# Optimization experiments

Measured on AMD Instinct MI355X. Metric: run time of the kernel, lower is better.

## Reference

```python
import jax, jax.numpy as jnp
import numpy as np

B, H, W, DIM, HEADS, WS, SHIFT, MLP_RATIO = 32, 56, 56, 256, 8, 7, 3, 4
N = WS * WS                      # tokens per window = 49
NW = (H // WS) * (W // WS)       # windows per image = 64
HEAD_DIM = DIM // HEADS
HIDDEN = DIM * MLP_RATIO


def _rel_index():
    # standard Swin relative position index, shape (N, N), values in [0, (2*WS-1)^2)
    coords = np.stack(np.meshgrid(np.arange(WS), np.arange(WS), indexing='ij')).reshape(2, -1)
    rel = (coords[:, :, None] - coords[:, None, :]).transpose(1, 2, 0)
    rel[:, :, 0] += WS - 1
    rel[:, :, 1] += WS - 1
    rel[:, :, 0] *= 2 * WS - 1
    return rel.sum(-1).astype(np.int32)


def _attn_mask():
    # shifted-window attention mask, shape (NW, N, N), values in {0, -100}
    img = np.zeros((H, W))
    slices = (slice(0, -WS), slice(-WS, -SHIFT), slice(-SHIFT, None))
    cnt = 0
    for hs in slices:
        for ws_ in slices:
            img[hs, ws_] = cnt
            cnt += 1
    mw = img.reshape(H // WS, WS, W // WS, WS).transpose(0, 2, 1, 3).reshape(-1, N)
    diff = mw[:, None, :] - mw[:, :, None]
    return np.where(diff != 0, -100.0, 0.0).astype(np.float32)


def setup_inputs() -> dict:
    key = jax.random.key(0)
    ks = jax.random.split(key, 16)
    s = 0.02
    return {
        'x': jax.random.normal(ks[0], (B, H * W, DIM), jnp.float32),
        'norm1_w': jnp.ones((DIM,), jnp.float32),
        'norm1_b': jnp.zeros((DIM,), jnp.float32),
        'qkv_w': jax.random.normal(ks[1], (3 * DIM, DIM), jnp.float32) * s,
        'qkv_b': jnp.zeros((3 * DIM,), jnp.float32),
        'rpb_table': jax.random.normal(ks[2], ((2 * WS - 1) ** 2, HEADS), jnp.float32) * s,
        'proj_w': jax.random.normal(ks[3], (DIM, DIM), jnp.float32) * s,
        'proj_b': jnp.zeros((DIM,), jnp.float32),
        'norm2_w': jnp.ones((DIM,), jnp.float32),
        'norm2_b': jnp.zeros((DIM,), jnp.float32),
        'fc1_w': jax.random.normal(ks[4], (HIDDEN, DIM), jnp.float32) * s,
        'fc1_b': jnp.zeros((HIDDEN,), jnp.float32),
        'fc2_w': jax.random.normal(ks[5], (DIM, HIDDEN), jnp.float32) * s,
        'fc2_b': jnp.zeros((DIM,), jnp.float32),
        'rel_idx': jnp.asarray(_rel_index()),
        'attn_mask': jnp.asarray(_attn_mask()),
    }


def _ln(t, w, b):
    mu = t.mean(-1, keepdims=True)
    var = ((t - mu) ** 2).mean(-1, keepdims=True)
    return (t - mu) * jax.lax.rsqrt(var + 1e-5) * w + b


def reference(x, norm1_w, norm1_b, qkv_w, qkv_b, rpb_table, proj_w, proj_b,
              norm2_w, norm2_b, fc1_w, fc1_b, fc2_w, fc2_b, rel_idx, attn_mask):
    Bz = x.shape[0]
    shortcut = x
    h = _ln(x, norm1_w, norm1_b).reshape(Bz, H, W, DIM)
    h = jnp.roll(h, (-SHIFT, -SHIFT), axis=(1, 2))                      # cyclic shift
    # window partition -> (Bz*NW, N, C)
    h = h.reshape(Bz, H // WS, WS, W // WS, WS, DIM).transpose(0, 1, 3, 2, 4, 5).reshape(-1, N, DIM)
    qkv = (h @ qkv_w.T + qkv_b).reshape(-1, N, 3, HEADS, HEAD_DIM).transpose(2, 0, 3, 1, 4)
    q, k, v = qkv[0], qkv[1], qkv[2]                                    # (Bz*NW, heads, N, d)
    scale = HEAD_DIM ** -0.5
    attn = jnp.einsum('whnd,whmd->whnm', q * scale, k)
    bias = rpb_table[rel_idx].transpose(2, 0, 1)                        # (heads, N, N)
    attn = attn + bias[None]
    attn = attn.reshape(Bz, NW, HEADS, N, N) + attn_mask[None, :, None]  # shift mask
    attn = jax.nn.softmax(attn.reshape(-1, HEADS, N, N), axis=-1)
    out = jnp.einsum('whnm,whmd->whnd', attn, v).transpose(0, 2, 1, 3).reshape(-1, N, DIM)
    out = out @ proj_w.T + proj_b
    # window reverse + un-shift
    out = out.reshape(Bz, H // WS, W // WS, WS, WS, DIM).transpose(0, 1, 3, 2, 4, 5).reshape(Bz, H, W, DIM)
    out = jnp.roll(out, (SHIFT, SHIFT), axis=(1, 2)).reshape(Bz, H * W, DIM)
    x = shortcut + out
    # residual MLP (pre-LN), exact GELU as in nn.GELU default
    h2 = _ln(x, norm2_w, norm2_b)
    h2 = jax.nn.gelu(h2 @ fc1_w.T + fc1_b, approximate=False)
    return x + (h2 @ fc2_w.T + fc2_b)
```

## Files before the change

### kernel.cpp

```cpp
#include <hip/hip_runtime.h>

typedef unsigned short ushort_t;
typedef __attribute__((ext_vector_type(8))) __bf16 bf16x8;
typedef __attribute__((ext_vector_type(4))) float floatx4;

#define TOKS 100352

__device__ __forceinline__ ushort_t f2bf(float f) {
    union { float f; unsigned u; } a; a.f = f;
    unsigned r = a.u + 0x7fffu + ((a.u >> 16) & 1u);
    return (ushort_t)(r >> 16);
}
__device__ __forceinline__ float bf2f(ushort_t u) {
    union { unsigned v; float f; } a; a.v = ((unsigned)u) << 16; return a.f;
}

__device__ __forceinline__ void async16(const void* g, void* l) {
    __builtin_amdgcn_global_load_lds(
        (const __attribute__((address_space(1))) unsigned int*)g,
        (__attribute__((address_space(3))) unsigned int*)l,
        16, 0, 0);
}

__device__ __forceinline__ int win_to_orig(int t) {
    int b = t / 3136, rr = t - b * 3136;
    int w_ = rr / 49, pos = rr - w_ * 49;
    int wi = w_ >> 3, wj = w_ & 7;
    int ti = pos / 7, tj = pos - ti * 7;
    int h = wi * 7 + ti + 3; if (h >= 56) h -= 56;
    int w = wj * 7 + tj + 3; if (w >= 56) w -= 56;
    return b * 3136 + h * 56 + w;
}

__global__ void convert_kernel(const float* __restrict__ qkv_w, const float* __restrict__ proj_w,
                               const float* __restrict__ fc1_w, const float* __restrict__ fc2_w,
                               const float* __restrict__ rpb, const int* __restrict__ rel_idx,
                               const float* __restrict__ amask, const float* __restrict__ qkv_b,
                               ushort_t* __restrict__ wq, ushort_t* __restrict__ wp,
                               ushort_t* __restrict__ w1, ushort_t* __restrict__ w2,
                               float* __restrict__ bmF, float* __restrict__ qb2) {
    const float scale = 0.17677669529663687f;
    int i = blockIdx.x * 256 + threadIdx.x;
    if (i < 196608) { float v = qkv_w[i]; wq[i] = f2bf(i < 65536 ? v * scale : v); }
    if (i < 65536)  wp[i] = f2bf(proj_w[i]);
    if (i < 262144) { w1[i] = f2bf(fc1_w[i]); w2[i] = f2bf(fc2_w[i]); }
    if (i < 768)    qb2[i] = qkv_b[i] * (i < 256 ? scale : 1.f);
    if (i < 2097152) {
        int r = i & 3, lane = (i >> 2) & 63, t = (i >> 8) & 15, wh = i >> 12;
        int head = wh & 7, wimg = wh >> 3;
        int mi = t >> 2, nj = t & 3;
        int quad = lane >> 4, l15 = lane & 15;
        int ii = mi * 16 + quad * 4 + r, jj = nj * 16 + l15;
        float val = -1e30f;
        if (ii < 49 && jj < 49)
            val = rpb[rel_idx[ii * 49 + jj] * 8 + head] + amask[wimg * 2401 + ii * 49 + jj];
        bmF[i] = val;
    }
}

__global__ __launch_bounds__(256) void ln_kernel(const float* __restrict__ xin,
                                                 const float* __restrict__ gw,
                                                 const float* __restrict__ gb,
                                                 ushort_t* __restrict__ outb) {
    const int wid = threadIdx.x >> 6, lane = threadIdx.x & 63;
    const int t_out = blockIdx.x * 4 + wid;
    const int t_in = win_to_orig(t_out);
    const float4* src = (const float4*)(xin + (long)t_in * 256);
    float4 v = src[lane];
    float s  = v.x + v.y + v.z + v.w;
    float s2 = v.x*v.x + v.y*v.y + v.z*v.z + v.w*v.w;
    #pragma unroll
    for (int d = 32; d >= 1; d >>= 1) { s += __shfl_xor(s, d, 64); s2 += __shfl_xor(s2, d, 64); }
    float mu  = s * 0.00390625f;
    float var = s2 * 0.00390625f - mu * mu;
    float ry  = rsqrtf(var + 1e-5f);
    float4 w4 = ((const float4*)gw)[lane], b4 = ((const float4*)gb)[lane];
    unsigned long long p =
          (unsigned long long)f2bf((v.x - mu) * ry * w4.x + b4.x)
        | ((unsigned long long)f2bf((v.y - mu) * ry * w4.y + b4.y) << 16)
        | ((unsigned long long)f2bf((v.z - mu) * ry * w4.z + b4.z) << 32)
        | ((unsigned long long)f2bf((v.w - mu) * ry * w4.w + b4.w) << 48);
    ((unsigned long long*)(outb + (long)t_out * 256))[lane] = p;
}

template <int MODE, int N_LD, int KD, int CT>
__global__ __launch_bounds__(256, 2) void gemm_kernel(const ushort_t* __restrict__ A,
                                                      const ushort_t* __restrict__ Bw,
                                                      const float* __restrict__ bias,
                                                      void* __restrict__ outp,
                                                      const ushort_t* __restrict__ x1w,
                                                      int rowOff) {
    __shared__ __align__(16) ushort_t As[2][128 * 32];
    __shared__ __align__(16) ushort_t Bs[2][128 * 32];
    const int tid = threadIdx.x;
    const int lane = tid & 63;
    const int wid = tid >> 6;
    const int wm = wid & 1, wn = wid >> 1;
    const int l15 = lane & 15, quad = lane >> 4;
    const int v = blockIdx.x;
    const int j = v >> 3;
    const long tileM = (long)((j / CT) * 8 + (v & 7)) * 128;
    const long tileN = (long)(j % CT) * 128;

    floatx4 acc[4][4];
    #pragma unroll
    for (int i = 0; i < 4; i++)
        #pragma unroll
        for (int jj = 0; jj < 4; jj++) acc[i][jj] = {0.f, 0.f, 0.f, 0.f};

    const int o1 = tid * 16;
    const int r1 = o1 >> 6, c1 = (o1 & 63) >> 1;
    const int lo = o1 >> 1;
    const ushort_t* Ar1 = A + (tileM + r1) * KD + c1;
    const ushort_t* Ar2 = A + (tileM + r1 + 64) * KD + c1;
    const ushort_t* Br1 = Bw + (tileN + r1) * KD + c1;
    const ushort_t* Br2 = Bw + (tileN + r1 + 64) * KD + c1;

    async16(Ar1, &As[0][lo]);
    async16(Ar2, &As[0][lo + 2048]);
    async16(Br1, &Bs[0][lo]);
    async16(Br2, &Bs[0][lo + 2048]);

    #pragma unroll
    for (int it = 0; it < KD / 32; ++it) {
        const int buf = it & 1, nbuf = buf ^ 1;
        const int k0 = it * 32;
        if (it + 1 < KD / 32) {
            async16(Ar1 + k0 + 32, &As[nbuf][lo]);
            async16(Ar2 + k0 + 32, &As[nbuf][lo + 2048]);
            async16(Br1 + k0 + 32, &Bs[nbuf][lo]);
            async16(Br2 + k0 + 32, &Bs[nbuf][lo + 2048]);
            asm volatile("s_waitcnt vmcnt(4)" ::: "memory");
        } else {
            asm volatile("s_waitcnt vmcnt(0)" ::: "memory");
        }
        __builtin_amdgcn_s_barrier();
        bf16x8 af[4], bfr[4];
        #pragma unroll
        for (int mi = 0; mi < 4; mi++)
            af[mi] = *(const bf16x8*)&As[buf][(wm * 64 + mi * 16 + l15) * 32 + quad * 8];
        #pragma unroll
        for (int nj = 0; nj < 4; nj++)
            bfr[nj] = *(const bf16x8*)&Bs[buf][(wn * 64 + nj * 16 + l15) * 32 + quad * 8];
        #pragma unroll
        for (int mi = 0; mi < 4; mi++)
            #pragma unroll
            for (int nj = 0; nj < 4; nj++)
                acc[mi][nj] = __builtin_amdgcn_mfma_f32_16x16x32_bf16(af[mi], bfr[nj], acc[mi][nj], 0, 0, 0);
        __builtin_amdgcn_sched_barrier(0);
        __builtin_amdgcn_s_barrier();
    }

    #pragma unroll
    for (int mi = 0; mi < 4; mi++)
      #pragma unroll
      for (int nj = 0; nj < 4; nj++)
        #pragma unroll
        for (int r = 0; r < 4; r++) {
            long row = tileM + wm * 64 + mi * 16 + quad * 4 + r;
            long col = tileN + wn * 64 + nj * 16 + l15;
            float val = acc[mi][nj][r] + bias[col];
            if (MODE == 0) {
                ((ushort_t*)outp)[row * N_LD + col] = f2bf(val);
            } else if (MODE == 2) {
                float g = 0.5f * val * (1.f + erff(val * 0.70710678118654752f));
                ((ushort_t*)outp)[row * N_LD + col] = f2bf(g);
            } else {
                float res = bf2f(x1w[row * 256 + col]);
                int orig = win_to_orig((int)row + rowOff);
                ((float*)outp)[(long)orig * 256 + col] = val + res;
            }
        }
}

__global__ __launch_bounds__(256, 2) void proj_ln_kernel(
        const ushort_t* __restrict__ A, const ushort_t* __restrict__ Bw,
        const float* __restrict__ pb, const float* __restrict__ x_res,
        const float* __restrict__ n2w, const float* __restrict__ n2b,
        ushort_t* __restrict__ x1w, ushort_t* __restrict__ h2out) {
    __shared__ __align__(16) ushort_t As[2][64 * 32];
    __shared__ __align__(16) ushort_t Bs[2][256 * 32];
    __shared__ float red_s[4][64];
    __shared__ float red_q[4][64];
    const int tid = threadIdx.x, lane = tid & 63, wid = tid >> 6;
    const int l15 = lane & 15, quad = lane >> 4;
    const long tileM = (long)blockIdx.x * 64;

    floatx4 acc[4][4];
    #pragma unroll
    for (int i = 0; i < 4; i++)
        #pragma unroll
        for (int j = 0; j < 4; j++) acc[i][j] = {0.f, 0.f, 0.f, 0.f};

    const int oA = tid * 16;
    const int rA = oA >> 6, cA = (oA & 63) >> 1;
    const ushort_t* Ap = A + (tileM + rA) * 256 + cA;

    async16(Ap, &As[0][oA >> 1]);
    #pragma unroll
    for (int ch = 0; ch < 4; ch++) {
        int o = ch * 4096 + oA;
        async16(Bw + (o >> 6) * 256 + ((o & 63) >> 1), &Bs[0][o >> 1]);
    }

    #pragma unroll
    for (int it = 0; it < 8; ++it) {
        const int buf = it & 1, nbuf = buf ^ 1;
        const int k0 = it * 32;
        if (it + 1 < 8) {
            async16(Ap + k0 + 32, &As[nbuf][oA >> 1]);
            #pragma unroll
            for (int ch = 0; ch < 4; ch++) {
                int o = ch * 4096 + oA;
                async16(Bw + (o >> 6) * 256 + ((o & 63) >> 1) + k0 + 32, &Bs[nbuf][o >> 1]);
            }
            asm volatile("s_waitcnt vmcnt(5)" ::: "memory");
        } else {
            asm volatile("s_waitcnt vmcnt(0)" ::: "memory");
        }
        __builtin_amdgcn_s_barrier();
        bf16x8 af[4], bfr[4];
        #pragma unroll
        for (int mi = 0; mi < 4; mi++)
            af[mi] = *(const bf16x8*)&As[buf][(mi * 16 + l15) * 32 + quad * 8];
        #pragma unroll
        for (int nj = 0; nj < 4; nj++)
            bfr[nj] = *(const bf16x8*)&Bs[buf][(wid * 64 + nj * 16 + l15) * 32 + quad * 8];
        #pragma unroll
        for (int mi = 0; mi < 4; mi++)
            #pragma unroll
            for (int nj = 0; nj < 4; nj++)
                acc[mi][nj] = __builtin_amdgcn_mfma_f32_16x16x32_bf16(af[mi], bfr[nj], acc[mi][nj], 0, 0, 0);
        __builtin_amdgcn_sched_barrier(0);
        __builtin_amdgcn_s_barrier();
    }

    #pragma unroll
    for (int mi = 0; mi < 4; mi++)
      #pragma unroll
      for (int r = 0; r < 4; r++) {
        int iloc = mi * 16 + quad * 4 + r;
        int orig = win_to_orig((int)tileM + iloc);
        float s = 0.f, q = 0.f;
        #pragma unroll
        for (int nj = 0; nj < 4; nj++) {
            int col = wid * 64 + nj * 16 + l15;
            float val = acc[mi][nj][r] + pb[col] + x_res[(long)orig * 256 + col];
            x1w[(tileM + iloc) * 256 + col] = f2bf(val);
            acc[mi][nj][r] = val;
            s += val; q += val * val;
        }
        #pragma unroll
        for (int d = 1; d < 16; d <<= 1) { s += __shfl_xor(s, d, 64); q += __shfl_xor(q, d, 64); }
        if (l15 == 0) { red_s[wid][iloc] = s; red_q[wid][iloc] = q; }
      }
    __syncthreads();
    #pragma unroll
    for (int mi = 0; mi < 4; mi++)
      #pragma unroll
      for (int r = 0; r < 4; r++) {
        int iloc = mi * 16 + quad * 4 + r;
        float s = red_s[0][iloc] + red_s[1][iloc] + red_s[2][iloc] + red_s[3][iloc];
        float q = red_q[0][iloc] + red_q[1][iloc] + red_q[2][iloc] + red_q[3][iloc];
        float mu = s * 0.00390625f;
        float var = q * 0.00390625f - mu * mu;
        float rstd = rsqrtf(var + 1e-5f);
        #pragma unroll
        for (int nj = 0; nj < 4; nj++) {
            int col = wid * 64 + nj * 16 + l15;
            float val = acc[mi][nj][r];
            h2out[(tileM + iloc) * 256 + col] = f2bf((val - mu) * rstd * n2w[col] + n2b[col]);
        }
      }
}

__global__ __launch_bounds__(256) void attn_kernel(const ushort_t* __restrict__ qkv,
                                                   const float* __restrict__ bmF,
                                                   ushort_t* __restrict__ attnout) {
    __shared__ __align__(16) ushort_t lds[4 * 5832];
    const int tid = threadIdx.x, lane = tid & 63, wid = tid >> 6;
    ushort_t* Pl = &lds[wid * 5832];
    ushort_t* Vt = Pl + 49 * 72;
    const int whid = blockIdx.x * 4 + wid;
    const int win = whid >> 3, head = whid & 7;
    const int l15 = lane & 15, quad = lane >> 4;
    const long base = (long)win * 49 * 768;

    const floatx4* bmc = (const floatx4*)bmF
                       + ((long)((win & 63) * 8 + head) * 16) * 64 + lane;
    floatx4 S[4][4];
    #pragma unroll
    for (int mi = 0; mi < 4; mi++)
        #pragma unroll
        for (int nj = 0; nj < 4; nj++)
            S[mi][nj] = bmc[(mi * 4 + nj) * 64];

    bf16x8 qf[4], kf[4];
    #pragma unroll
    for (int t4 = 0; t4 < 4; t4++) {
        int tok = t4 * 16 + l15; if (tok > 48) tok = 48;
        const ushort_t* p = qkv + base + (long)tok * 768 + head * 32 + quad * 8;
        qf[t4] = *(const bf16x8*)p;
        kf[t4] = *(const bf16x8*)(p + 256);
    }

    const int jl = lane;
    const int jc = jl < 49 ? jl : 48;
    const uint4* vsrc = (const uint4*)(qkv + base + (long)jc * 768 + 512 + head * 32);
    uint4 vz; vz.x = vz.y = vz.z = vz.w = 0u;
    uint4 vv[4];
    #pragma unroll
    for (int q4 = 0; q4 < 4; q4++) vv[q4] = (jl < 49) ? vsrc[q4] : vz;

    #pragma unroll
    for (int mi = 0; mi < 4; mi++)
        #pragma unroll
        for (int nj = 0; nj < 4; nj++)
            S[mi][nj] = __builtin_amdgcn_mfma_f32_16x16x32_bf16(qf[mi], kf[nj], S[mi][nj], 0, 0, 0);

    #pragma unroll
    for (int q4 = 0; q4 < 4; q4++) {
        int db = q4 * 8;
        uint4 v4 = vv[q4];
        Vt[(db+0)*72 + jl] = (ushort_t)v4.x;  Vt[(db+1)*72 + jl] = (ushort_t)(v4.x >> 16);
        Vt[(db+2)*72 + jl] = (ushort_t)v4.y;  Vt[(db+3)*72 + jl] = (ushort_t)(v4.y >> 16);
        Vt[(db+4)*72 + jl] = (ushort_t)v4.z;  Vt[(db+5)*72 + jl] = (ushort_t)(v4.z >> 16);
        Vt[(db+6)*72 + jl] = (ushort_t)v4.w;  Vt[(db+7)*72 + jl] = (ushort_t)(v4.w >> 16);
    }

    float rinv[4][4];
    #pragma unroll
    for (int mi = 0; mi < 4; mi++)
      #pragma unroll
      for (int r = 0; r < 4; r++) {
          float m = fmaxf(fmaxf(S[mi][0][r], S[mi][1][r]), fmaxf(S[mi][2][r], S[mi][3][r]));
          #pragma unroll
          for (int d = 1; d < 16; d <<= 1) m = fmaxf(m, __shfl_xor(m, d, 64));
          float e[4], sum = 0.f;
          #pragma unroll
          for (int nj = 0; nj < 4; nj++) { e[nj] = __expf(S[mi][nj][r] - m); sum += e[nj]; }
          #pragma unroll
          for (int d = 1; d < 16; d <<= 1) sum += __shfl_xor(sum, d, 64);
          rinv[mi][r] = 1.f / sum;
          int i = mi * 16 + quad * 4 + r;
          if (i < 49) {
              #pragma unroll
              for (int nj = 0; nj < 4; nj++) Pl[i * 72 + (nj * 16 + l15)] = f2bf(e[nj]);
          }
      }


    floatx4 O[4][2];
    #pragma unroll
    for (int mi = 0; mi < 4; mi++) { O[mi][0] = {0.f,0.f,0.f,0.f}; O[mi][1] = {0.f,0.f,0.f,0.f}; }
    #pragma unroll
    for (int kc = 0; kc < 2; kc++) {
        bf16x8 pf[4], vf[2];
        #pragma unroll
        for (int mi = 0; mi < 4; mi++) {
            int pr = mi * 16 + l15; if (pr > 48) pr = 48;
            pf[mi] = *(const bf16x8*)&Pl[pr * 72 + kc * 32 + quad * 8];
        }
        #pragma unroll
        for (int n2 = 0; n2 < 2; n2++)
            vf[n2] = *(const bf16x8*)&Vt[(n2 * 16 + l15) * 72 + kc * 32 + quad * 8];
        #pragma unroll
        for (int mi = 0; mi < 4; mi++)
            #pragma unroll
            for (int n2 = 0; n2 < 2; n2++)
                O[mi][n2] = __builtin_amdgcn_mfma_f32_16x16x32_bf16(pf[mi], vf[n2], O[mi][n2], 0, 0, 0);
    }

    #pragma unroll
    for (int mi = 0; mi < 4; mi++)
      #pragma unroll
      for (int n2 = 0; n2 < 2; n2++)
        #pragma unroll
        for (int r = 0; r < 4; r++) {
            int i = mi * 16 + quad * 4 + r;
            if (i < 49) {
                long orow = ((long)win * 49 + i) * 256 + head * 32 + n2 * 16 + l15;
                attnout[orow] = f2bf(O[mi][n2][r] * rinv[mi][r]);
            }
        }
}

extern "C" void kernel_launch(void* const* d_in, const int* in_sizes, int n_in,
                              void* d_out, int out_size, void* d_ws, size_t ws_size,
                              hipStream_t stream) {
    const float* x      = (const float*)d_in[0];
    const float* n1w    = (const float*)d_in[1];
    const float* n1b    = (const float*)d_in[2];
    const float* qkv_w  = (const float*)d_in[3];
    const float* qkv_b  = (const float*)d_in[4];
    const float* rpb    = (const float*)d_in[5];
    const float* proj_w = (const float*)d_in[6];
    const float* proj_b = (const float*)d_in[7];
    const float* n2w    = (const float*)d_in[8];
    const float* n2b    = (const float*)d_in[9];
    const float* fc1_w  = (const float*)d_in[10];
    const float* fc1_b  = (const float*)d_in[11];
    const float* fc2_w  = (const float*)d_in[12];
    const float* fc2_b  = (const float*)d_in[13];
    const int*   rel_idx= (const int*)d_in[14];
    const float* amask  = (const float*)d_in[15];

    char* ws = (char*)d_ws;
    ushort_t* wq   = (ushort_t*)(ws + 0);
    ushort_t* wp   = (ushort_t*)(ws + 393216);
    ushort_t* w1   = (ushort_t*)(ws + 524288);
    ushort_t* w2   = (ushort_t*)(ws + 1048576);
    ushort_t* hwin = (ushort_t*)(ws + 1572864);
    ushort_t* qkvb = (ushort_t*)(ws + 52953088);
    ushort_t* h2   = (ushort_t*)(ws + 104333312);
    ushort_t* x1w  = (ushort_t*)(ws + 155713536);
    ushort_t* h3   = hwin;
    float* bmF = (float*)d_out;
    float* qb2 = (float*)((char*)d_out + 8388608);

    convert_kernel<<<8192, 256, 0, stream>>>(qkv_w, proj_w, fc1_w, fc2_w, rpb, rel_idx,
                                             amask, qkv_b, wq, wp, w1, w2, bmF, qb2);
    ln_kernel<<<TOKS / 4, 256, 0, stream>>>(x, n1w, n1b, hwin);
    gemm_kernel<0, 768, 256, 6><<<4704, 256, 0, stream>>>(hwin, wq, qb2, qkvb, nullptr, 0);
    attn_kernel<<<4096, 256, 0, stream>>>(qkvb, bmF, hwin);
    proj_ln_kernel<<<1568, 256, 0, stream>>>(hwin, wp, proj_b, x, n2w, n2b, x1w, h2);
    for (int c = 0; c < 2; c++) {
        gemm_kernel<2, 1024, 256, 8><<<3136, 256, 0, stream>>>(
            h2 + (long)c * 50176 * 256, w1, fc1_b, h3, nullptr, 0);
        gemm_kernel<4, 256, 1024, 2><<<784, 256, 0, stream>>>(
            h3, w2, fc2_b, (float*)d_out, x1w + (long)c * 50176 * 256, c * 50176);
    }
    (void)in_sizes; (void)n_in; (void)out_size; (void)ws_size;
}
```

Baseline: 623.6 us.

## Fuse MLP fc1, GELU and fc2 into one kernel keeping hidden tile in LDS

```diff
diff --git a/kernel.cpp b/kernel.cpp
--- a/kernel.cpp
+++ b/kernel.cpp
@@ -87,9 +87,7 @@
 __global__ __launch_bounds__(256, 2) void gemm_kernel(const ushort_t* __restrict__ A,
                                                       const ushort_t* __restrict__ Bw,
                                                       const float* __restrict__ bias,
-                                                      void* __restrict__ outp,
-                                                      const ushort_t* __restrict__ x1w,
-                                                      int rowOff) {
+                                                      void* __restrict__ outp) {
     __shared__ __align__(16) ushort_t As[2][128 * 32];
     __shared__ __align__(16) ushort_t Bs[2][128 * 32];
     const int tid = threadIdx.x;
@@ -160,16 +158,7 @@
             long row = tileM + wm * 64 + mi * 16 + quad * 4 + r;
             long col = tileN + wn * 64 + nj * 16 + l15;
             float val = acc[mi][nj][r] + bias[col];
-            if (MODE == 0) {
-                ((ushort_t*)outp)[row * N_LD + col] = f2bf(val);
-            } else if (MODE == 2) {
-                float g = 0.5f * val * (1.f + erff(val * 0.70710678118654752f));
-                ((ushort_t*)outp)[row * N_LD + col] = f2bf(g);
-            } else {
-                float res = bf2f(x1w[row * 256 + col]);
-                int orig = win_to_orig((int)row + rowOff);
-                ((float*)outp)[(long)orig * 256 + col] = val + res;
-            }
+            ((ushort_t*)outp)[row * N_LD + col] = f2bf(val);
         }
 }
 
@@ -270,6 +259,155 @@
             int col = wid * 64 + nj * 16 + l15;
             float val = acc[mi][nj][r];
             h2out[(tileM + iloc) * 256 + col] = f2bf((val - mu) * rstd * n2w[col] + n2b[col]);
+        }
+      }
+}
+
+__global__ __launch_bounds__(256, 2) void mlp_kernel(
+        const ushort_t* __restrict__ A,
+        const ushort_t* __restrict__ w1,
+        const ushort_t* __restrict__ w2,
+        const float* __restrict__ b1,
+        const float* __restrict__ b2,
+        const ushort_t* __restrict__ x1w,
+        float* __restrict__ outp) {
+    __shared__ __align__(16) ushort_t As[2][64 * 32];
+    __shared__ __align__(16) ushort_t Bs[2][256 * 32];
+    __shared__ __align__(16) ushort_t H3[64 * 264];
+    const int tid = threadIdx.x, lane = tid & 63, wid = tid >> 6;
+    const int l15 = lane & 15, quad = lane >> 4;
+    const long tileM = (long)blockIdx.x * 64;
+
+    const int oA = tid * 16;
+    const int rA = oA >> 6, cA = (oA & 63) >> 1;
+    const ushort_t* Ap = A + (tileM + rA) * 256 + cA;
+
+    floatx4 acc2[4][4];
+    #pragma unroll
+    for (int i = 0; i < 4; i++)
+        #pragma unroll
+        for (int j = 0; j < 4; j++) acc2[i][j] = {0.f, 0.f, 0.f, 0.f};
+
+    async16(Ap, &As[0][oA >> 1]);
+    #pragma unroll
+    for (int ch = 0; ch < 4; ch++) {
+        int o = ch * 4096 + oA;
+        async16(w1 + (long)(o >> 6) * 256 + ((o & 63) >> 1), &Bs[0][o >> 1]);
+    }
+
+    for (int c = 0; c < 4; ++c) {
+        floatx4 acc1[4][4];
+        #pragma unroll
+        for (int i = 0; i < 4; i++)
+            #pragma unroll
+            for (int j = 0; j < 4; j++) acc1[i][j] = {0.f, 0.f, 0.f, 0.f};
+
+        #pragma unroll
+        for (int it = 0; it < 8; ++it) {
+            const int buf = it & 1, nbuf = buf ^ 1;
+            const int k0 = it * 32;
+            if (it < 7) {
+                async16(Ap + k0 + 32, &As[nbuf][oA >> 1]);
+                #pragma unroll
+                for (int ch = 0; ch < 4; ch++) {
+                    int o = ch * 4096 + oA;
+                    async16(w1 + (long)(c * 256 + (o >> 6)) * 256 + ((o & 63) >> 1) + k0 + 32,
+                            &Bs[nbuf][o >> 1]);
+                }
+                asm volatile("s_waitcnt vmcnt(5)" ::: "memory");
+            } else {
+                #pragma unroll
+                for (int ch = 0; ch < 4; ch++) {
+                    int o = ch * 4096 + oA;
+                    async16(w2 + (long)(o >> 6) * 1024 + c * 256 + ((o & 63) >> 1), &Bs[0][o >> 1]);
+                }
+                asm volatile("s_waitcnt vmcnt(4)" ::: "memory");
+            }
+            __builtin_amdgcn_s_barrier();
+            bf16x8 af[4], bfr[4];
+            #pragma unroll
+            for (int mi = 0; mi < 4; mi++)
+                af[mi] = *(const bf16x8*)&As[buf][(mi * 16 + l15) * 32 + quad * 8];
+            #pragma unroll
+            for (int nj = 0; nj < 4; nj++)
+                bfr[nj] = *(const bf16x8*)&Bs[buf][(wid * 64 + nj * 16 + l15) * 32 + quad * 8];
+            #pragma unroll
+            for (int mi = 0; mi < 4; mi++)
+                #pragma unroll
+                for (int nj = 0; nj < 4; nj++)
+                    acc1[mi][nj] = __builtin_amdgcn_mfma_f32_16x16x32_bf16(af[mi], bfr[nj], acc1[mi][nj], 0, 0, 0);
+            __builtin_amdgcn_sched_barrier(0);
+            __builtin_amdgcn_s_barrier();
+        }
+
+        #pragma unroll
+        for (int mi = 0; mi < 4; mi++)
+          #pragma unroll
+          for (int nj = 0; nj < 4; nj++)
+            #pragma unroll
+            for (int r = 0; r < 4; r++) {
+                int row = mi * 16 + quad * 4 + r;
+                int col = wid * 64 + nj * 16 + l15;
+                float val = acc1[mi][nj][r] + b1[c * 256 + col];
+                float g = 0.5f * val * (1.f + erff(val * 0.70710678118654752f));
+                H3[row * 264 + col] = f2bf(g);
+            }
+        asm volatile("s_waitcnt lgkmcnt(0)" ::: "memory");
+        __builtin_amdgcn_s_barrier();
+
+        #pragma unroll
+        for (int it = 0; it < 8; ++it) {
+            const int buf = it & 1, nbuf = buf ^ 1;
+            const int k0 = it * 32;
+            if (it < 7) {
+                #pragma unroll
+                for (int ch = 0; ch < 4; ch++) {
+                    int o = ch * 4096 + oA;
+                    async16(w2 + (long)(o >> 6) * 1024 + c * 256 + ((o & 63) >> 1) + k0 + 32,
+                            &Bs[nbuf][o >> 1]);
+                }
+                asm volatile("s_waitcnt vmcnt(4)" ::: "memory");
+            } else if (c < 3) {
+                async16(Ap, &As[0][oA >> 1]);
+                #pragma unroll
+                for (int ch = 0; ch < 4; ch++) {
+                    int o = ch * 4096 + oA;
+                    async16(w1 + (long)((c + 1) * 256 + (o >> 6)) * 256 + ((o & 63) >> 1),
+                            &Bs[0][o >> 1]);
+                }
+                asm volatile("s_waitcnt vmcnt(5)" ::: "memory");
+            } else {
+                asm volatile("s_waitcnt vmcnt(0)" ::: "memory");
+            }
+            __builtin_amdgcn_s_barrier();
+            bf16x8 af[4], bfr[4];
+            #pragma unroll
+            for (int mi = 0; mi < 4; mi++)
+                af[mi] = *(const bf16x8*)&H3[(mi * 16 + l15) * 264 + k0 + quad * 8];
+            #pragma unroll
+            for (int nj = 0; nj < 4; nj++)
+                bfr[nj] = *(const bf16x8*)&Bs[buf][(wid * 64 + nj * 16 + l15) * 32 + quad * 8];
+            #pragma unroll
+            for (int mi = 0; mi < 4; mi++)
+                #pragma unroll
+                for (int nj = 0; nj < 4; nj++)
+                    acc2[mi][nj] = __builtin_amdgcn_mfma_f32_16x16x32_bf16(af[mi], bfr[nj], acc2[mi][nj], 0, 0, 0);
+            __builtin_amdgcn_sched_barrier(0);
+            __builtin_amdgcn_s_barrier();
+        }
+    }
+
+    #pragma unroll
+    for (int mi = 0; mi < 4; mi++)
+      #pragma unroll
+      for (int r = 0; r < 4; r++) {
+        int iloc = mi * 16 + quad * 4 + r;
+        int orig = win_to_orig((int)tileM + iloc);
+        #pragma unroll
+        for (int nj = 0; nj < 4; nj++) {
+            int col = wid * 64 + nj * 16 + l15;
+            float val = acc2[mi][nj][r] + b2[col] + bf2f(x1w[(tileM + iloc) * 256 + col]);
+            outp[(long)orig * 256 + col] = val;
         }
       }
 }
@@ -414,21 +552,15 @@
     ushort_t* qkvb = (ushort_t*)(ws + 52953088);
     ushort_t* h2   = (ushort_t*)(ws + 104333312);
     ushort_t* x1w  = (ushort_t*)(ws + 155713536);
-    ushort_t* h3   = hwin;
     float* bmF = (float*)d_out;
     float* qb2 = (float*)((char*)d_out + 8388608);
 
     convert_kernel<<<8192, 256, 0, stream>>>(qkv_w, proj_w, fc1_w, fc2_w, rpb, rel_idx,
                                              amask, qkv_b, wq, wp, w1, w2, bmF, qb2);
     ln_kernel<<<TOKS / 4, 256, 0, stream>>>(x, n1w, n1b, hwin);
-    gemm_kernel<0, 768, 256, 6><<<4704, 256, 0, stream>>>(hwin, wq, qb2, qkvb, nullptr, 0);
+    gemm_kernel<0, 768, 256, 6><<<4704, 256, 0, stream>>>(hwin, wq, qb2, qkvb);
     attn_kernel<<<4096, 256, 0, stream>>>(qkvb, bmF, hwin);
     proj_ln_kernel<<<1568, 256, 0, stream>>>(hwin, wp, proj_b, x, n2w, n2b, x1w, h2);
-    for (int c = 0; c < 2; c++) {
-        gemm_kernel<2, 1024, 256, 8><<<3136, 256, 0, stream>>>(
-            h2 + (long)c * 50176 * 256, w1, fc1_b, h3, nullptr, 0);
-        gemm_kernel<4, 256, 1024, 2><<<784, 256, 0, stream>>>(
-            h3, w2, fc2_b, (float*)d_out, x1w + (long)c * 50176 * 256, c * 50176);
-    }
+    mlp_kernel<<<1568, 256, 0, stream>>>(h2, w1, w2, fc1_b, fc2_b, x1w, (float*)d_out);
     (void)in_sizes; (void)n_in; (void)out_size; (void)ws_size;
 }
```

Measured after the change: 651.9 us. +4.5%, slower.

## Double GEMM K-tile to 64 with XOR-swizzled LDS layout

Applied to the files above, without the earlier changes.

```diff
diff --git a/kernel.cpp b/kernel.cpp
--- a/kernel.cpp
+++ b/kernel.cpp
@@ -90,8 +90,8 @@
                                                       void* __restrict__ outp,
                                                       const ushort_t* __restrict__ x1w,
                                                       int rowOff) {
-    __shared__ __align__(16) ushort_t As[2][128 * 32];
-    __shared__ __align__(16) ushort_t Bs[2][128 * 32];
+    __shared__ __align__(16) ushort_t As[2][128 * 64];
+    __shared__ __align__(16) ushort_t Bs[2][128 * 64];
     const int tid = threadIdx.x;
     const int lane = tid & 63;
     const int wid = tid >> 6;
@@ -108,45 +108,53 @@
         #pragma unroll
         for (int jj = 0; jj < 4; jj++) acc[i][jj] = {0.f, 0.f, 0.f, 0.f};
 
-    const int o1 = tid * 16;
-    const int r1 = o1 >> 6, c1 = (o1 & 63) >> 1;
-    const int lo = o1 >> 1;
-    const ushort_t* Ar1 = A + (tileM + r1) * KD + c1;
-    const ushort_t* Ar2 = A + (tileM + r1 + 64) * KD + c1;
-    const ushort_t* Br1 = Bw + (tileN + r1) * KD + c1;
-    const ushort_t* Br2 = Bw + (tileN + r1 + 64) * KD + c1;
-
-    async16(Ar1, &As[0][lo]);
-    async16(Ar2, &As[0][lo + 2048]);
-    async16(Br1, &Bs[0][lo]);
-    async16(Br2, &Bs[0][lo + 2048]);
-
-    #pragma unroll
-    for (int it = 0; it < KD / 32; ++it) {
+    const int rloc = tid >> 3;
+    const int cs = (((tid & 7) ^ (rloc & 7)) * 8);
+    const ushort_t* Ar = A + (tileM + rloc) * KD + cs;
+    const ushort_t* Br = Bw + (tileN + rloc) * KD + cs;
+    const int dst = tid * 16;
+
+    #pragma unroll
+    for (int rj = 0; rj < 4; rj++) {
+        async16(Ar + (long)rj * 32 * KD, (char*)As[0] + rj * 4096 + dst);
+        async16(Br + (long)rj * 32 * KD, (char*)Bs[0] + rj * 4096 + dst);
+    }
+
+    constexpr int NPH = KD / 64;
+    #pragma unroll
+    for (int it = 0; it < NPH; ++it) {
         const int buf = it & 1, nbuf = buf ^ 1;
-        const int k0 = it * 32;
-        if (it + 1 < KD / 32) {
-            async16(Ar1 + k0 + 32, &As[nbuf][lo]);
-            async16(Ar2 + k0 + 32, &As[nbuf][lo + 2048]);
-            async16(Br1 + k0 + 32, &Bs[nbuf][lo]);
-            async16(Br2 + k0 + 32, &Bs[nbuf][lo + 2048]);
-            asm volatile("s_waitcnt vmcnt(4)" ::: "memory");
+        if (it + 1 < NPH) {
+            const int k0n = (it + 1) * 64;
+            #pragma unroll
+            for (int rj = 0; rj < 4; rj++) {
+                async16(Ar + (long)rj * 32 * KD + k0n, (char*)As[nbuf] + rj * 4096 + dst);
+                async16(Br + (long)rj * 32 * KD + k0n, (char*)Bs[nbuf] + rj * 4096 + dst);
+            }
+            asm volatile("s_waitcnt vmcnt(8)" ::: "memory");
         } else {
             asm volatile("s_waitcnt vmcnt(0)" ::: "memory");
         }
         __builtin_amdgcn_s_barrier();
-        bf16x8 af[4], bfr[4];
-        #pragma unroll
-        for (int mi = 0; mi < 4; mi++)
-            af[mi] = *(const bf16x8*)&As[buf][(wm * 64 + mi * 16 + l15) * 32 + quad * 8];
-        #pragma unroll
-        for (int nj = 0; nj < 4; nj++)
-            bfr[nj] = *(const bf16x8*)&Bs[buf][(wn * 64 + nj * 16 + l15) * 32 + quad * 8];
-        #pragma unroll
-        for (int mi = 0; mi < 4; mi++)
-            #pragma unroll
-            for (int nj = 0; nj < 4; nj++)
-                acc[mi][nj] = __builtin_amdgcn_mfma_f32_16x16x32_bf16(af[mi], bfr[nj], acc[mi][nj], 0, 0, 0);
+        #pragma unroll
+        for (int kk = 0; kk < 2; kk++) {
+            bf16x8 af[4], bfr[4];
+            #pragma unroll
+            for (int mi = 0; mi < 4; mi++) {
+                int row = wm * 64 + mi * 16 + l15;
+                af[mi] = *(const bf16x8*)&As[buf][row * 64 + (((kk * 4 + quad) ^ (row & 7)) * 8)];
+            }
+            #pragma unroll
+            for (int nj = 0; nj < 4; nj++) {
+                int row = wn * 64 + nj * 16 + l15;
+                bfr[nj] = *(const bf16x8*)&Bs[buf][row * 64 + (((kk * 4 + quad) ^ (row & 7)) * 8)];
+            }
+            #pragma unroll
+            for (int mi = 0; mi < 4; mi++)
+                #pragma unroll
+                for (int nj = 0; nj < 4; nj++)
+                    acc[mi][nj] = __builtin_amdgcn_mfma_f32_16x16x32_bf16(af[mi], bfr[nj], acc[mi][nj], 0, 0, 0);
+        }
         __builtin_amdgcn_sched_barrier(0);
         __builtin_amdgcn_s_barrier();
     }
```

After: 640.6 us. 2.7% more time.

## Triple-buffer LDS staging with prefetch distance two in GEMM kernels

Applied to the files above, without the earlier changes.

```diff
diff --git a/kernel.cpp b/kernel.cpp
--- a/kernel.cpp
+++ b/kernel.cpp
@@ -90,8 +90,8 @@
                                                       void* __restrict__ outp,
                                                       const ushort_t* __restrict__ x1w,
                                                       int rowOff) {
-    __shared__ __align__(16) ushort_t As[2][128 * 32];
-    __shared__ __align__(16) ushort_t Bs[2][128 * 32];
+    __shared__ __align__(16) ushort_t As[3][128 * 32];
+    __shared__ __align__(16) ushort_t Bs[3][128 * 32];
     const int tid = threadIdx.x;
     const int lane = tid & 63;
     const int wid = tid >> 6;
@@ -101,6 +101,7 @@
     const int j = v >> 3;
     const long tileM = (long)((j / CT) * 8 + (v & 7)) * 128;
     const long tileN = (long)(j % CT) * 128;
+    constexpr int NPH = KD / 32;
 
     floatx4 acc[4][4];
     #pragma unroll
@@ -116,25 +117,31 @@
     const ushort_t* Br1 = Bw + (tileN + r1) * KD + c1;
     const ushort_t* Br2 = Bw + (tileN + r1 + 64) * KD + c1;
 
-    async16(Ar1, &As[0][lo]);
-    async16(Ar2, &As[0][lo + 2048]);
-    async16(Br1, &Bs[0][lo]);
-    async16(Br2, &Bs[0][lo + 2048]);
-
-    #pragma unroll
-    for (int it = 0; it < KD / 32; ++it) {
-        const int buf = it & 1, nbuf = buf ^ 1;
-        const int k0 = it * 32;
-        if (it + 1 < KD / 32) {
-            async16(Ar1 + k0 + 32, &As[nbuf][lo]);
-            async16(Ar2 + k0 + 32, &As[nbuf][lo + 2048]);
-            async16(Br1 + k0 + 32, &Bs[nbuf][lo]);
-            async16(Br2 + k0 + 32, &Bs[nbuf][lo + 2048]);
+    #pragma unroll
+    for (int p = 0; p < 2; p++) {
+        async16(Ar1 + p * 32, &As[p][lo]);
+        async16(Ar2 + p * 32, &As[p][lo + 2048]);
+        async16(Br1 + p * 32, &Bs[p][lo]);
+        async16(Br2 + p * 32, &Bs[p][lo + 2048]);
+    }
+
+    #pragma unroll
+    for (int it = 0; it < NPH; ++it) {
+        const int buf = it % 3;
+        if (it + 1 < NPH) {
             asm volatile("s_waitcnt vmcnt(4)" ::: "memory");
         } else {
             asm volatile("s_waitcnt vmcnt(0)" ::: "memory");
         }
         __builtin_amdgcn_s_barrier();
+        if (it + 2 < NPH) {
+            const int nb = (it + 2) % 3;
+            const int k2 = (it + 2) * 32;
+            async16(Ar1 + k2, &As[nb][lo]);
+            async16(Ar2 + k2, &As[nb][lo + 2048]);
+            async16(Br1 + k2, &Bs[nb][lo]);
+            async16(Br2 + k2, &Bs[nb][lo + 2048]);
+        }
         bf16x8 af[4], bfr[4];
         #pragma unroll
         for (int mi = 0; mi < 4; mi++)
@@ -147,8 +154,6 @@
             #pragma unroll
             for (int nj = 0; nj < 4; nj++)
                 acc[mi][nj] = __builtin_amdgcn_mfma_f32_16x16x32_bf16(af[mi], bfr[nj], acc[mi][nj], 0, 0, 0);
-        __builtin_amdgcn_sched_barrier(0);
-        __builtin_amdgcn_s_barrier();
     }
 
     #pragma unroll
@@ -178,8 +183,8 @@
         const float* __restrict__ pb, const float* __restrict__ x_res,
         const float* __restrict__ n2w, const float* __restrict__ n2b,
         ushort_t* __restrict__ x1w, ushort_t* __restrict__ h2out) {
-    __shared__ __align__(16) ushort_t As[2][64 * 32];
-    __shared__ __align__(16) ushort_t Bs[2][256 * 32];
+    __shared__ __align__(16) ushort_t As[3][64 * 32];
+    __shared__ __align__(16) ushort_t Bs[3][256 * 32];
     __shared__ float red_s[4][64];
     __shared__ float red_q[4][64];
     const int tid = threadIdx.x, lane = tid & 63, wid = tid >> 6;
@@ -196,29 +201,35 @@
     const int rA = oA >> 6, cA = (oA & 63) >> 1;
     const ushort_t* Ap = A + (tileM + rA) * 256 + cA;
 
-    async16(Ap, &As[0][oA >> 1]);
-    #pragma unroll
-    for (int ch = 0; ch < 4; ch++) {
-        int o = ch * 4096 + oA;
-        async16(Bw + (o >> 6) * 256 + ((o & 63) >> 1), &Bs[0][o >> 1]);
+    #pragma unroll
+    for (int p = 0; p < 2; p++) {
+        async16(Ap + p * 32, &As[p][oA >> 1]);
+        #pragma unroll
+        for (int ch = 0; ch < 4; ch++) {
+            int o = ch * 4096 + oA;
+            async16(Bw + (o >> 6) * 256 + ((o & 63) >> 1) + p * 32, &Bs[p][o >> 1]);
+        }
     }
 
     #pragma unroll
     for (int it = 0; it < 8; ++it) {
-        const int buf = it & 1, nbuf = buf ^ 1;
-        const int k0 = it * 32;
+        const int buf = it % 3;
         if (it + 1 < 8) {
-            async16(Ap + k0 + 32, &As[nbuf][oA >> 1]);
+            asm volatile("s_waitcnt vmcnt(5)" ::: "memory");
+        } else {
+            asm volatile("s_waitcnt vmcnt(0)" ::: "memory");
+        }
+        __builtin_amdgcn_s_barrier();
+        if (it + 2 < 8) {
+            const int nb = (it + 2) % 3;
+            const int k2 = (it + 2) * 32;
+            async16(Ap + k2, &As[nb][oA >> 1]);
             #pragma unroll
             for (int ch = 0; ch < 4; ch++) {
                 int o = ch * 4096 + oA;
-                async16(Bw + (o >> 6) * 256 + ((o & 63) >> 1) + k0 + 32, &Bs[nbuf][o >> 1]);
+                async16(Bw + (o >> 6) * 256 + ((o & 63) >> 1) + k2, &Bs[nb][o >> 1]);
             }
-            asm volatile("s_waitcnt vmcnt(5)" ::: "memory");
-        } else {
-            asm volatile("s_waitcnt vmcnt(0)" ::: "memory");
-        }
-        __builtin_amdgcn_s_barrier();
+        }
         bf16x8 af[4], bfr[4];
         #pragma unroll
         for (int mi = 0; mi < 4; mi++)
@@ -231,8 +242,6 @@
             #pragma unroll
             for (int nj = 0; nj < 4; nj++)
                 acc[mi][nj] = __builtin_amdgcn_mfma_f32_16x16x32_bf16(af[mi], bfr[nj], acc[mi][nj], 0, 0, 0);
-        __builtin_amdgcn_sched_barrier(0);
-        __builtin_amdgcn_s_barrier();
     }
 
     #pragma unroll
```

Result: slower. 688.1 us (+10.3%).
